# Kernel optimization log

Hardware: AMD Instinct MI355X
Metric: run time of the kernel (lower is better)

## Reference

```python
import jax, jax.numpy as jnp
import numpy as np

OUT_H, OUT_W = 256, 256  # output_size init kwarg


def setup_inputs() -> dict:
    key = jax.random.key(0)
    k1, k2 = jax.random.split(key)
    X = jax.random.normal(k1, (16, 512, 512, 16), dtype=jnp.float32)
    theta = jax.random.normal(k2, (16, 6), dtype=jnp.float32)
    return {"X": X, "theta": theta}


def reference(X, theta):
    B, H, W, C = X.shape
    N = OUT_H * OUT_W

    # regular grid in [-1,1]^2 with homogeneous coordinate, shape [3, N]
    xs = jnp.linspace(-1.0, 1.0, OUT_W)
    ys = jnp.linspace(-1.0, 1.0, OUT_H)
    xc, yc = jnp.meshgrid(xs, ys)  # [OUT_H, OUT_W]
    grid = jnp.stack([xc.ravel(), yc.ravel(), jnp.ones(N, dtype=jnp.float32)], axis=0)

    # apply affine transform: [B,2,3] @ [3,N] -> [B,2,N]
    T = theta.reshape(B, 2, 3)
    sg = jnp.einsum('bij,jn->bin', T, grid)

    # map from [-1,1] to pixel coords (note: scaled by W/H, not W-1/H-1, as in source)
    x = 0.5 * (sg[:, 0, :] + 1.0) * jnp.float32(W)  # [B, N]
    y = 0.5 * (sg[:, 1, :] + 1.0) * jnp.float32(H)

    x0 = x.astype(jnp.int32)  # truncation toward zero, matches K.cast
    x1 = x0 + 1
    y0 = y.astype(jnp.int32)
    y1 = y0 + 1
    x0 = jnp.clip(x0, 0, W - 1)
    x1 = jnp.clip(x1, 0, W - 1)
    y0 = jnp.clip(y0, 0, H - 1)
    y1 = jnp.clip(y1, 0, H - 1)

    flat = X.reshape(B, H * W, C)

    def gather(yi, xi):
        idx = yi * W + xi  # [B, N]
        return jnp.take_along_axis(flat, idx[..., None], axis=1)  # [B, N, C]

    pa = gather(y0, x0)
    pb = gather(y1, x0)
    pc = gather(y0, x1)
    pd = gather(y1, x1)

    x0f = x0.astype(jnp.float32)
    x1f = x1.astype(jnp.float32)
    y0f = y0.astype(jnp.float32)
    y1f = y1.astype(jnp.float32)

    wa = ((x1f - x) * (y1f - y))[..., None]
    wb = ((x1f - x) * (y - y0f))[..., None]
    wc = ((x - x0f) * (y1f - y))[..., None]
    wd = ((x - x0f) * (y - y0f))[..., None]

    out = wa * pa + wb * pb + wc * pc + wd * pd  # [B, N, C]
    return out.reshape(B, OUT_H, OUT_W, C)
```

## Files before the change

### kernel.cpp

```cpp
#include <hip/hip_runtime.h>


#define IN_H 512
#define IN_W 512
#define OUT_HW_BITS 8
#define NCH 16

__global__ __launch_bounds__(256) void bilerp_kernel(
    const float* __restrict__ X,
    const float* __restrict__ theta,
    float* __restrict__ out)
{
    const int tid = blockIdx.x * blockDim.x + threadIdx.x;
    const int c4 = tid & 3;
    const int p  = tid >> 2;
    const int ox = p & 255;
    const int oy = (p >> OUT_HW_BITS) & 255;
    const int b  = p >> (2 * OUT_HW_BITS);

    const float xc = fmaf((float)ox, 2.0f / 255.0f, -1.0f);
    const float yc = fmaf((float)oy, 2.0f / 255.0f, -1.0f);

    const float* t = theta + b * 6;
    const float xs = fmaf(t[0], xc, fmaf(t[1], yc, t[2]));
    const float ys = fmaf(t[3], xc, fmaf(t[4], yc, t[5]));

    const float x = (xs + 1.0f) * 256.0f;
    const float y = (ys + 1.0f) * 256.0f;

    int x0 = (int)x;
    int y0 = (int)y;
    int x1 = x0 + 1;
    int y1 = y0 + 1;
    x0 = min(max(x0, 0), IN_W - 1);
    x1 = min(max(x1, 0), IN_W - 1);
    y0 = min(max(y0, 0), IN_H - 1);
    y1 = min(max(y1, 0), IN_H - 1);

    const float x0f = (float)x0, x1f = (float)x1;
    const float y0f = (float)y0, y1f = (float)y1;
    const float wa = (x1f - x) * (y1f - y);
    const float wb = (x1f - x) * (y - y0f);
    const float wc = (x - x0f) * (y1f - y);
    const float wd = (x - x0f) * (y - y0f);

    const float4* Xb = (const float4*)(X + (size_t)b * (IN_H * IN_W * NCH));
    const int ia = (y0 * IN_W + x0) * 4 + c4;
    const int ib = (y1 * IN_W + x0) * 4 + c4;
    const int ic = (y0 * IN_W + x1) * 4 + c4;
    const int id = (y1 * IN_W + x1) * 4 + c4;

    const float4 pa = Xb[ia];
    const float4 pb = Xb[ib];
    const float4 pc = Xb[ic];
    const float4 pd = Xb[id];

    float4 o;
    o.x = fmaf(wa, pa.x, fmaf(wb, pb.x, fmaf(wc, pc.x, wd * pd.x)));
    o.y = fmaf(wa, pa.y, fmaf(wb, pb.y, fmaf(wc, pc.y, wd * pd.y)));
    o.z = fmaf(wa, pa.z, fmaf(wb, pb.z, fmaf(wc, pc.z, wd * pd.z)));
    o.w = fmaf(wa, pa.w, fmaf(wb, pb.w, fmaf(wc, pc.w, wd * pd.w)));

    ((float4*)out)[tid] = o;
}

extern "C" void kernel_launch(void* const* d_in, const int* in_sizes, int n_in,
                              void* d_out, int out_size, void* d_ws, size_t ws_size,
                              hipStream_t stream) {
    const float* X     = (const float*)d_in[0];
    const float* theta = (const float*)d_in[1];
    float* out = (float*)d_out;

    const int total = 16 * 256 * 256 * 4;
    const int block = 256;
    const int grid = total / block;
    bilerp_kernel<<<grid, block, 0, stream>>>(X, theta, out);
}
```

Baseline: 334.5 us.

## Tile output into 8x8 pixel blocks with XCD-aware block remap and nontemporal stores

Each block now covers an 8x8 square of output pixels instead of 64 pixels along one row, so the four bilinear taps of neighbouring threads fall on a compact 2D region of the input and share cache lines. Block IDs are remapped so that consecutive tiles go to the same XCD slab, which keeps L2 locality on the multi-die chip. Output writes use nontemporal stores so they do not evict input lines from cache. Output writes now come from 8-pixel row segments rather than full contiguous blocks, which makes them less coalesced.

```diff
diff --git a/kernel.cpp b/kernel.cpp
--- a/kernel.cpp
+++ b/kernel.cpp
@@ -3,27 +3,39 @@
 
 #define IN_H 512
 #define IN_W 512
-#define OUT_HW_BITS 8
 #define NCH 16
+
+typedef float v4f __attribute__((ext_vector_type(4)));
 
 __global__ __launch_bounds__(256) void bilerp_kernel(
     const float* __restrict__ X,
     const float* __restrict__ theta,
     float* __restrict__ out)
 {
-    const int tid = blockIdx.x * blockDim.x + threadIdx.x;
-    const int c4 = tid & 3;
-    const int p  = tid >> 2;
-    const int ox = p & 255;
-    const int oy = (p >> OUT_HW_BITS) & 255;
-    const int b  = p >> (2 * OUT_HW_BITS);
+    const int G = gridDim.x;
+    const int slab = G >> 3;
+    const int bid = blockIdx.x;
+    const int eff = (bid & 7) * slab + (bid >> 3);
+
+    const int b    = eff >> 10;
+    const int tile = eff & 1023;
+    const int tx   = tile & 31;
+    const int ty   = tile >> 5;
+
+    const int t  = threadIdx.x;
+    const int c4 = t & 3;
+    const int px = (t >> 2) & 7;
+    const int py = t >> 5;
+
+    const int ox = (tx << 3) + px;
+    const int oy = (ty << 3) + py;
 
     const float xc = fmaf((float)ox, 2.0f / 255.0f, -1.0f);
     const float yc = fmaf((float)oy, 2.0f / 255.0f, -1.0f);
 
-    const float* t = theta + b * 6;
-    const float xs = fmaf(t[0], xc, fmaf(t[1], yc, t[2]));
-    const float ys = fmaf(t[3], xc, fmaf(t[4], yc, t[5]));
+    const float* th = theta + b * 6;
+    const float xs = fmaf(th[0], xc, fmaf(th[1], yc, th[2]));
+    const float ys = fmaf(th[3], xc, fmaf(th[4], yc, th[5]));
 
     const float x = (xs + 1.0f) * 256.0f;
     const float y = (ys + 1.0f) * 256.0f;
@@ -44,24 +56,25 @@
     const float wc = (x - x0f) * (y1f - y);
     const float wd = (x - x0f) * (y - y0f);
 
-    const float4* Xb = (const float4*)(X + (size_t)b * (IN_H * IN_W * NCH));
+    const v4f* Xb = (const v4f*)(X + (size_t)b * (IN_H * IN_W * NCH));
     const int ia = (y0 * IN_W + x0) * 4 + c4;
     const int ib = (y1 * IN_W + x0) * 4 + c4;
     const int ic = (y0 * IN_W + x1) * 4 + c4;
     const int id = (y1 * IN_W + x1) * 4 + c4;
 
-    const float4 pa = Xb[ia];
-    const float4 pb = Xb[ib];
-    const float4 pc = Xb[ic];
-    const float4 pd = Xb[id];
+    const v4f pa = Xb[ia];
+    const v4f pb = Xb[ib];
+    const v4f pc = Xb[ic];
+    const v4f pd = Xb[id];
 
-    float4 o;
+    v4f o;
     o.x = fmaf(wa, pa.x, fmaf(wb, pb.x, fmaf(wc, pc.x, wd * pd.x)));
     o.y = fmaf(wa, pa.y, fmaf(wb, pb.y, fmaf(wc, pc.y, wd * pd.y)));
     o.z = fmaf(wa, pa.z, fmaf(wb, pb.z, fmaf(wc, pc.z, wd * pd.z)));
     o.w = fmaf(wa, pa.w, fmaf(wb, pb.w, fmaf(wc, pc.w, wd * pd.w)));
 
-    ((float4*)out)[tid] = o;
+    const int oidx = (((b << 8) + oy) << 8) * 4 + (ox << 2) + c4;
+    __builtin_nontemporal_store(o, (v4f*)out + oidx);
 }
 
 extern "C" void kernel_launch(void* const* d_in, const int* in_sizes, int n_in,
@@ -71,8 +84,6 @@
     const float* theta = (const float*)d_in[1];
     float* out = (float*)d_out;
 
-    const int total = 16 * 256 * 256 * 4;
-    const int block = 256;
-    const int grid = total / block;
-    bilerp_kernel<<<grid, block, 0, stream>>>(X, theta, out);
+    const int grid = 16 * 32 * 32;
+    bilerp_kernel<<<grid, 256, 0, stream>>>(X, theta, out);
 }
```

Result: no change. 334.0 us (-0.1%).
